# Kernel tuning notes

Measured on AMD Instinct MI355X. Metric: run time of the kernel, lower is better.

## Reference

```python
import jax, jax.numpy as jnp
import numpy as np

B, IN, H = 4096, 1024, 1024

def setup_inputs() -> dict:
    key = jax.random.key(0)
    ks = jax.random.split(key, 8)
    s = 1.0 / np.sqrt(IN + H)  # ~torch Linear init scale
    return {
        "x": jax.random.normal(ks[0], (B, IN), jnp.float32),
        "h_prev": jax.random.normal(ks[1], (B, H), jnp.float32),
        "c_prev": jax.random.normal(ks[2], (B, H), jnp.float32),
        "Wf": jax.random.normal(ks[3], (IN + H, H), jnp.float32) * s,
        "bf": jnp.zeros((H,), jnp.float32),
        "Wi": jax.random.normal(ks[4], (IN + H, H), jnp.float32) * s,
        "bi": jnp.zeros((H,), jnp.float32),
        "Wg": jax.random.normal(ks[5], (IN + H, H), jnp.float32) * s,
        "bg": jnp.zeros((H,), jnp.float32),
        "Wo": jax.random.normal(ks[6], (IN + H, H), jnp.float32) * s,
        "bo": jnp.zeros((H,), jnp.float32),
    }

def reference(x, h_prev, c_prev, Wf, bf, Wi, bi, Wg, bg, Wo, bo):
    combined = jnp.concatenate([x, h_prev], axis=1)          # [B, IN+H]
    # fuse the 4 gate projections into one GEMM: [B, IN+H] x [IN+H, 4H]
    W = jnp.concatenate([Wf, Wi, Wg, Wo], axis=1)            # [IN+H, 4H]
    b = jnp.concatenate([bf, bi, bg, bo], axis=0)            # [4H]
    gates = combined @ W + b                                  # [B, 4H]
    f_t, i_t, g_t, o_t = jnp.split(gates, 4, axis=1)
    f_t = jax.nn.sigmoid(f_t)
    i_t = jax.nn.sigmoid(i_t)
    g_t = jnp.tanh(g_t)
    o_t = jax.nn.sigmoid(o_t)
    c_next = f_t * c_prev + i_t * g_t
    h_next = o_t * jnp.tanh(c_next)
    return (h_next, c_next)
```

## Files before the change

### kernel.cpp

```cpp
#include <hip/hip_runtime.h>

#define B_DIM 4096
#define H_DIM 1024
#define K_DIM 2048
#define NTILE (K_DIM / 64)

typedef unsigned short u16;
typedef unsigned int u32;
typedef __attribute__((ext_vector_type(8))) short short8;
typedef __attribute__((ext_vector_type(4))) float f32x4;

typedef const __attribute__((address_space(1))) void* gas_ptr;
typedef __attribute__((address_space(3))) void* las_ptr;

#define WT_ELEMS (4 * H_DIM * K_DIM)
#define AC_ELEMS (B_DIM * K_DIM)
#define WS_NEEDED ((size_t)(WT_ELEMS + AC_ELEMS) * 2)

__device__ __forceinline__ void gl_lds16(const u16* g, u16* l) {
    __builtin_amdgcn_global_load_lds((gas_ptr)g, (las_ptr)l, 16, 0, 0);
}
__device__ __forceinline__ float bf2f(u16 v) {
    return __builtin_bit_cast(float, (u32)((u32)v << 16));
}
__device__ __forceinline__ u16 f2bf(float f) {
    u32 u = __builtin_bit_cast(u32, f);
    return (u16)((u + 0x7fffu + ((u >> 16) & 1u)) >> 16);
}
__device__ __forceinline__ float sigm(float x) { return 1.0f / (1.0f + __expf(-x)); }
__device__ __forceinline__ float tanh_f(float x) { return 1.0f - 2.0f / (__expf(2.0f * x) + 1.0f); }

__global__ __launch_bounds__(256) void prep_all(const float* __restrict__ x, const float* __restrict__ h,
                                                const float* __restrict__ Wf, const float* __restrict__ Wi,
                                                const float* __restrict__ Wg, const float* __restrict__ Wo,
                                                u16* __restrict__ A, u16* __restrict__ Wt) {
    const int t = threadIdx.x;
    if (blockIdx.x < 512) {
#pragma unroll
        for (int it = 0; it < 8; ++it) {
            int e = it * (512 * 256 * 8) + (blockIdx.x * 256 + t) * 8;
            int m = e >> 11, c = e & 2047;
            const float* src = (c < 1024) ? (x + (size_t)m * 1024 + c)
                                          : (h + (size_t)m * 1024 + (c - 1024));
            float4 v0 = ((const float4*)src)[0], v1 = ((const float4*)src)[1];
            short8 q;
            q[0] = (short)f2bf(v0.x); q[1] = (short)f2bf(v0.y); q[2] = (short)f2bf(v0.z); q[3] = (short)f2bf(v0.w);
            q[4] = (short)f2bf(v1.x); q[5] = (short)f2bf(v1.y); q[6] = (short)f2bf(v1.z); q[7] = (short)f2bf(v1.w);
            *(short8*)(A + e) = q;
        }
    } else {
        const int id = (blockIdx.x - 512) * 4 + (t >> 6);
        const int l = t & 63;
        const int k0 = (id & 31) * 64, n0 = ((id >> 5) & 15) * 64, g = id >> 9;
        const float* W = (g == 0) ? Wf : (g == 1) ? Wi : (g == 2) ? Wg : Wo;
        const int no = (l & 7) * 8;
        const int ko = (l >> 3) * 8;
        float f[8][8];
#pragma unroll
        for (int j = 0; j < 8; ++j) {
            const float4* s = (const float4*)(W + (size_t)(k0 + ko + j) * H_DIM + n0 + no);
            float4 a = s[0], b = s[1];
            f[j][0] = a.x; f[j][1] = a.y; f[j][2] = a.z; f[j][3] = a.w;
            f[j][4] = b.x; f[j][5] = b.y; f[j][6] = b.z; f[j][7] = b.w;
        }
        u16* dst0 = Wt + (size_t)g * ((size_t)H_DIM * K_DIM) + (size_t)(n0 + no) * K_DIM + k0 + ko;
#pragma unroll
        for (int w2 = 0; w2 < 8; ++w2) {
            short8 q;
#pragma unroll
            for (int j = 0; j < 8; ++j) q[j] = (short)f2bf(f[j][w2]);
            *(short8*)(dst0 + (size_t)w2 * K_DIM) = q;
        }
    }
}

#define PH_OPEN                                                  \
    __builtin_amdgcn_s_barrier();                                \
    __builtin_amdgcn_s_setprio(1)

#define PH_CLOSE                                                 \
    __builtin_amdgcn_s_setprio(0);                               \
    __builtin_amdgcn_s_barrier()

#define PH_CLOSE_VM2                                             \
    __builtin_amdgcn_s_setprio(0);                               \
    asm volatile("s_waitcnt vmcnt(2)" ::: "memory");             \
    __builtin_amdgcn_s_barrier()

#define PH_CLOSE_VM2_PIN                                         \
    __builtin_amdgcn_sched_barrier(0);                           \
    __builtin_amdgcn_s_setprio(0);                               \
    asm volatile("s_waitcnt vmcnt(2)" ::: "memory");             \
    __builtin_amdgcn_s_barrier()

#define PH_CLOSE_VM0                                             \
    __builtin_amdgcn_s_setprio(0);                               \
    asm volatile("s_waitcnt vmcnt(0)" ::: "memory");             \
    __builtin_amdgcn_s_barrier()

#define STG_A(NB, H)                                                              \
    gl_lds16(pa[H][0], &sm[NB][(H) * 8192 + t * 8]);        pa[H][0] += 64;       \
    gl_lds16(pa[H][1], &sm[NB][(H) * 8192 + 4096 + t * 8]); pa[H][1] += 64;

#define STG_B(NB, H)                                                                      \
    gl_lds16(pb[H][0], &sm[NB][16384 + (H) * 8192 + t * 8]);        pb[H][0] += 64;       \
    gl_lds16(pb[H][1], &sm[NB][16384 + (H) * 8192 + 4096 + t * 8]); pb[H][1] += 64;

#define RD_A(CB, KS)                                                                       \
    _Pragma("unroll") for (int mi = 0; mi < 8; ++mi)                                       \
        afr[mi] = *(const short8*)&sm[CB][(wr * 128 + mi * 16 + l15) * 64 +                \
                                          ((((KS) * 4 + quad) ^ v7) * 8)];

#define RD_B(CB, G, KS)                                                                    \
    (*(const short8*)&sm[CB][16384 + (G) * 4096 + (wc * 16 + l15) * 64 +                   \
                             ((((KS) * 4 + quad) ^ v7) * 8)])

#define MFMA_PAIR(GP)                                                                      \
    _Pragma("unroll") for (int mi = 0; mi < 8; ++mi)                                       \
        acc[mi][2 * (GP)] = __builtin_amdgcn_mfma_f32_16x16x32_bf16(                       \
            afr[mi], b0, acc[mi][2 * (GP)], 0, 0, 0);                                      \
    _Pragma("unroll") for (int mi = 0; mi < 8; ++mi)                                       \
        acc[mi][2 * (GP) + 1] = __builtin_amdgcn_mfma_f32_16x16x32_bf16(                   \
            afr[mi], b1, acc[mi][2 * (GP) + 1], 0, 0, 0);

__global__ __launch_bounds__(512, 2) void lstm_gemm(
    const u16* __restrict__ A, const u16* __restrict__ Wt, const float* __restrict__ c_prev,
    const float* __restrict__ bf_, const float* __restrict__ bi_,
    const float* __restrict__ bg_, const float* __restrict__ bo_,
    float* __restrict__ out) {
    __shared__ u16 sm[2][32768];

    const int t = threadIdx.x;
    const int w = t >> 6;
    const int l = t & 63;
    const int quad = l >> 4;
    const int l15 = l & 15;
    const int v7 = l15 & 7;
    const int wr = w >> 2;
    const int wc = w & 3;
    const int m0 = blockIdx.x * 256;
    const int j0 = blockIdx.y * 64;

    f32x4 acc[8][4];
#pragma unroll
    for (int mi = 0; mi < 8; ++mi)
#pragma unroll
        for (int g = 0; g < 4; ++g)
            acc[mi][g] = (f32x4){0.f, 0.f, 0.f, 0.f};

    const u16* pa[2][2];
    const u16* pb[2][2];
#pragma unroll
    for (int h = 0; h < 2; ++h)
#pragma unroll
        for (int i = 0; i < 2; ++i) {
            int e = h * 8192 + (i * 512 + t) * 8;
            int m = e >> 6, sl = (e >> 3) & 7;
            pa[h][i] = A + (size_t)(m0 + m) * K_DIM + ((sl ^ (m & 7)) * 8);
            int g = e >> 12, n = (e >> 6) & 63;
            pb[h][i] = Wt + (size_t)g * ((size_t)H_DIM * K_DIM) + (size_t)(j0 + n) * K_DIM +
                       ((sl ^ (n & 7)) * 8);
        }

    short8 afr[8], b0, b1;

    STG_A(0, 0); STG_A(0, 1); STG_B(0, 0); STG_B(0, 1);
    asm volatile("s_waitcnt vmcnt(2)" ::: "memory");
    __builtin_amdgcn_s_barrier();

    for (int kt = 0; kt < NTILE - 1; ++kt) {
        const int cb = kt & 1, nb = cb ^ 1;
        RD_A(cb, 0);
        b0 = RD_B(cb, 0, 0); b1 = RD_B(cb, 1, 0);
        STG_A(nb, 0);
        PH_OPEN;
        MFMA_PAIR(0);
        PH_CLOSE_VM2;
        b0 = RD_B(cb, 2, 0); b1 = RD_B(cb, 3, 0);
        STG_A(nb, 1);
        PH_OPEN;
        MFMA_PAIR(1);
        PH_CLOSE;
        RD_A(cb, 1);
        b0 = RD_B(cb, 0, 1); b1 = RD_B(cb, 1, 1);
        STG_B(nb, 0);
        PH_OPEN;
        MFMA_PAIR(0);
        PH_CLOSE;
        b0 = RD_B(cb, 2, 1); b1 = RD_B(cb, 3, 1);
        STG_B(nb, 1);
        PH_OPEN;
        MFMA_PAIR(1);
        PH_CLOSE_VM2_PIN;
    }
    {
        const int cb = (NTILE - 1) & 1;
        RD_A(cb, 0);
        b0 = RD_B(cb, 0, 0); b1 = RD_B(cb, 1, 0);
        PH_OPEN;
        MFMA_PAIR(0);
        PH_CLOSE_VM0;
        b0 = RD_B(cb, 2, 0); b1 = RD_B(cb, 3, 0);
        PH_OPEN;
        MFMA_PAIR(1);
        PH_CLOSE;
        RD_A(cb, 1);
        b0 = RD_B(cb, 0, 1); b1 = RD_B(cb, 1, 1);
        PH_OPEN;
        MFMA_PAIR(0);
        PH_CLOSE;
        b0 = RD_B(cb, 2, 1); b1 = RD_B(cb, 3, 1);
        MFMA_PAIR(1);
    }

    const int col = j0 + wc * 16 + l15;
    const float bF = bf_[col], bI = bi_[col], bG = bg_[col], bO = bo_[col];
#pragma unroll
    for (int mi = 0; mi < 8; ++mi) {
        const int rowbase = m0 + wr * 128 + mi * 16 + quad * 4;
        float cp[4];
#pragma unroll
        for (int rr = 0; rr < 4; ++rr)
            cp[rr] = c_prev[(size_t)(rowbase + rr) * H_DIM + col];
#pragma unroll
        for (int rr = 0; rr < 4; ++rr) {
            float fv = sigm(acc[mi][0][rr] + bF);
            float iv = sigm(acc[mi][1][rr] + bI);
            float gv = tanh_f(acc[mi][2][rr] + bG);
            float ov = sigm(acc[mi][3][rr] + bO);
            float cn = fv * cp[rr] + iv * gv;
            float hn = ov * tanh_f(cn);
            size_t idx = (size_t)(rowbase + rr) * H_DIM + col;
            out[idx] = hn;
            out[(size_t)B_DIM * H_DIM + idx] = cn;
        }
    }
}

__global__ __launch_bounds__(256) void lstm_f32(
    const float* __restrict__ x, const float* __restrict__ h_prev, const float* __restrict__ c_prev,
    const float* __restrict__ Wf, const float* __restrict__ Wi, const float* __restrict__ Wg, const float* __restrict__ Wo,
    const float* __restrict__ bf_, const float* __restrict__ bi_, const float* __restrict__ bg_, const float* __restrict__ bo_,
    float* __restrict__ out) {
    __shared__ u16 smem[16384];
    u16* sA = smem;
    u16* sB = smem + 4096;

    const int t = threadIdx.x;
    const int w = t >> 6;
    const int l = t & 63;
    const int quad = l >> 4;
    const int l15 = l & 15;
    const int wr = w >> 1;
    const int wc = w & 1;
    const int m0 = blockIdx.x * 128;
    const int j0 = blockIdx.y * 32;

    const int arow = t >> 1;
    const int akh = (t & 1) * 16;
    const int r7 = t & 127;
    const int bk = r7 >> 2;
    const int bn8 = (r7 & 3) * 8;
    const int kswz = ((((bk >> 3) ^ (bn8 >> 3)) << 3) | (bk & 7));
    const float* WpA = (t < 128) ? Wf : Wi;
    const float* WpB = (t < 128) ? Wg : Wo;
    const int gA = (t >> 7);
    const int gB = 2 + (t >> 7);

    f32x4 acc[2][4][2];
#pragma unroll
    for (int gi = 0; gi < 2; ++gi)
#pragma unroll
        for (int mi = 0; mi < 4; ++mi)
#pragma unroll
            for (int ni = 0; ni < 2; ++ni)
                acc[gi][mi][ni] = (f32x4){0.f, 0.f, 0.f, 0.f};

    for (int kt = 0; kt < K_DIM / 32; ++kt) {
        const float* srcA = (kt < 32) ? x : h_prev;
        const int koff = (kt & 31) * 32;
        __syncthreads();

        const float4* ap = (const float4*)(srcA + (size_t)(m0 + arow) * H_DIM + koff + akh);
        float4 a0 = ap[0], a1 = ap[1], a2 = ap[2], a3 = ap[3];
        short8 p0, p1;
        p0[0] = (short)f2bf(a0.x); p0[1] = (short)f2bf(a0.y); p0[2] = (short)f2bf(a0.z); p0[3] = (short)f2bf(a0.w);
        p0[4] = (short)f2bf(a1.x); p0[5] = (short)f2bf(a1.y); p0[6] = (short)f2bf(a1.z); p0[7] = (short)f2bf(a1.w);
        p1[0] = (short)f2bf(a2.x); p1[1] = (short)f2bf(a2.y); p1[2] = (short)f2bf(a2.z); p1[3] = (short)f2bf(a2.w);
        p1[4] = (short)f2bf(a3.x); p1[5] = (short)f2bf(a3.y); p1[6] = (short)f2bf(a3.z); p1[7] = (short)f2bf(a3.w);
        *(short8*)(sA + arow * 32 + akh) = p0;
        *(short8*)(sA + arow * 32 + akh + 8) = p1;

        const float* gpA = WpA + (size_t)(kt * 32 + bk) * H_DIM + j0 + bn8;
        const float* gpB = WpB + (size_t)(kt * 32 + bk) * H_DIM + j0 + bn8;
        float4 c0 = *(const float4*)gpA, c1 = *(const float4*)(gpA + 4);
        float4 d0 = *(const float4*)gpB, d1 = *(const float4*)(gpB + 4);
        sB[gA * 1024 + (bn8 + 0) * 32 + kswz] = f2bf(c0.x);
        sB[gA * 1024 + (bn8 + 1) * 32 + kswz] = f2bf(c0.y);
        sB[gA * 1024 + (bn8 + 2) * 32 + kswz] = f2bf(c0.z);
        sB[gA * 1024 + (bn8 + 3) * 32 + kswz] = f2bf(c0.w);
        sB[gA * 1024 + (bn8 + 4) * 32 + kswz] = f2bf(c1.x);
        sB[gA * 1024 + (bn8 + 5) * 32 + kswz] = f2bf(c1.y);
        sB[gA * 1024 + (bn8 + 6) * 32 + kswz] = f2bf(c1.z);
        sB[gA * 1024 + (bn8 + 7) * 32 + kswz] = f2bf(c1.w);
        sB[gB * 1024 + (bn8 + 0) * 32 + kswz] = f2bf(d0.x);
        sB[gB * 1024 + (bn8 + 1) * 32 + kswz] = f2bf(d0.y);
        sB[gB * 1024 + (bn8 + 2) * 32 + kswz] = f2bf(d0.z);
        sB[gB * 1024 + (bn8 + 3) * 32 + kswz] = f2bf(d0.w);
        sB[gB * 1024 + (bn8 + 4) * 32 + kswz] = f2bf(d1.x);
        sB[gB * 1024 + (bn8 + 5) * 32 + kswz] = f2bf(d1.y);
        sB[gB * 1024 + (bn8 + 6) * 32 + kswz] = f2bf(d1.z);
        sB[gB * 1024 + (bn8 + 7) * 32 + kswz] = f2bf(d1.w);
        __syncthreads();

        short8 bfr[2][2];
#pragma unroll
        for (int gi = 0; gi < 2; ++gi) {
            int g = wc * 2 + gi;
#pragma unroll
            for (int ni = 0; ni < 2; ++ni) {
                int n = ni * 16 + l15;
                bfr[gi][ni] = *(const short8*)(sB + g * 1024 + n * 32 + ((quad ^ (n >> 3)) * 8));
            }
        }
#pragma unroll
        for (int mi = 0; mi < 4; ++mi) {
            int m = wr * 64 + mi * 16 + l15;
            short8 afr = *(const short8*)(sA + m * 32 + quad * 8);
#pragma unroll
            for (int gi = 0; gi < 2; ++gi)
#pragma unroll
                for (int ni = 0; ni < 2; ++ni)
                    acc[gi][mi][ni] =
                        __builtin_amdgcn_mfma_f32_16x16x32_bf16(afr, bfr[gi][ni], acc[gi][mi][ni], 0, 0, 0);
        }
    }

    __syncthreads();
#pragma unroll
    for (int gi = 0; gi < 2; ++gi) {
        int g = wc * 2 + gi;
        const float* bp = (g == 0) ? bf_ : (g == 1) ? bi_ : (g == 2) ? bg_ : bo_;
#pragma unroll
        for (int ni = 0; ni < 2; ++ni) {
            int col = ni * 16 + l15;
            float bias = bp[j0 + col];
#pragma unroll
            for (int mi = 0; mi < 4; ++mi)
#pragma unroll
                for (int rr = 0; rr < 4; ++rr) {
                    int row = wr * 64 + mi * 16 + quad * 4 + rr;
                    float v = acc[gi][mi][ni][rr] + bias;
                    v = (g == 2) ? tanh_f(v) : sigm(v);
                    smem[g * 4096 + row * 32 + col] = f2bf(v);
                }
        }
    }
    __syncthreads();

    const int col = t & 31;
    const int rb = t >> 5;
#pragma unroll
    for (int p = 0; p < 16; ++p) {
        int row = p * 8 + rb;
        float fv = bf2f(smem[0 * 4096 + row * 32 + col]);
        float iv = bf2f(smem[1 * 4096 + row * 32 + col]);
        float gv = bf2f(smem[2 * 4096 + row * 32 + col]);
        float ov = bf2f(smem[3 * 4096 + row * 32 + col]);
        size_t oidx = (size_t)(m0 + row) * H_DIM + j0 + col;
        float cp = c_prev[oidx];
        float cn = fv * cp + iv * gv;
        float hn = ov * tanh_f(cn);
        out[oidx] = hn;
        out[(size_t)B_DIM * H_DIM + oidx] = cn;
    }
}

extern "C" void kernel_launch(void* const* d_in, const int* in_sizes, int n_in,
                              void* d_out, int out_size, void* d_ws, size_t ws_size,
                              hipStream_t stream) {
    const float* x   = (const float*)d_in[0];
    const float* hp  = (const float*)d_in[1];
    const float* cp  = (const float*)d_in[2];
    const float* Wf  = (const float*)d_in[3];
    const float* bf_ = (const float*)d_in[4];
    const float* Wi  = (const float*)d_in[5];
    const float* bi_ = (const float*)d_in[6];
    const float* Wg  = (const float*)d_in[7];
    const float* bg_ = (const float*)d_in[8];
    const float* Wo  = (const float*)d_in[9];
    const float* bo_ = (const float*)d_in[10];

    if (ws_size >= WS_NEEDED) {
        u16* Wt = (u16*)d_ws;
        u16* Ac = (u16*)d_ws + WT_ELEMS;
        prep_all<<<dim3(1024), dim3(256), 0, stream>>>(x, hp, Wf, Wi, Wg, Wo, Ac, Wt);
        lstm_gemm<<<dim3(B_DIM / 256, H_DIM / 64), dim3(512), 0, stream>>>(
            Ac, Wt, cp, bf_, bi_, bg_, bo_, (float*)d_out);
    } else {
        lstm_f32<<<dim3(B_DIM / 128, H_DIM / 32), dim3(256), 0, stream>>>(
            x, hp, cp, Wf, Wi, Wg, Wo, bf_, bi_, bg_, bo_, (float*)d_out);
    }
}
```

Before: 197.8 us.

## Switch gate GEMM to 32x32x16 MFMA with 4x2 wave layout

Replaces the 16x16x32 bf16 MFMA tiling (2x4 waves, each owning 128 rows by 16 columns per gate) with 32x32x16 MFMA tiles (4x2 waves, each owning 64 rows by 32 columns per gate). The LDS read addressing, the B staging pointer layout and the epilogue row mapping change to match the 32x32 accumulator layout. The aim is to cut LDS fragment reads per MFMA and issue fewer, larger matrix instructions. It shifts register pressure and LDS bank-access patterns, and the swizzle now keys on l&7 rather than l15&7.

Measured after the change: 207.3 us. 1.05x slower.

```diff
diff --git a/kernel.cpp b/kernel.cpp
--- a/kernel.cpp
+++ b/kernel.cpp
@@ -9,6 +9,7 @@
 typedef unsigned int u32;
 typedef __attribute__((ext_vector_type(8))) short short8;
 typedef __attribute__((ext_vector_type(4))) float f32x4;
+typedef __attribute__((ext_vector_type(16))) float f32x16;
 
 typedef const __attribute__((address_space(1))) void* gas_ptr;
 typedef __attribute__((address_space(3))) void* las_ptr;
@@ -106,22 +107,26 @@
     gl_lds16(pb[H][0], &sm[NB][16384 + (H) * 8192 + t * 8]);        pb[H][0] += 64;       \
     gl_lds16(pb[H][1], &sm[NB][16384 + (H) * 8192 + 4096 + t * 8]); pb[H][1] += 64;
 
-#define RD_A(CB, KS)                                                                       \
-    _Pragma("unroll") for (int mi = 0; mi < 8; ++mi)                                       \
-        afr[mi] = *(const short8*)&sm[CB][(wr * 128 + mi * 16 + l15) * 64 +                \
-                                          ((((KS) * 4 + quad) ^ v7) * 8)];
-
-#define RD_B(CB, G, KS)                                                                    \
-    (*(const short8*)&sm[CB][16384 + (G) * 4096 + (wc * 16 + l15) * 64 +                   \
-                             ((((KS) * 4 + quad) ^ v7) * 8)])
-
-#define MFMA_PAIR(GP)                                                                      \
-    _Pragma("unroll") for (int mi = 0; mi < 8; ++mi)                                       \
-        acc[mi][2 * (GP)] = __builtin_amdgcn_mfma_f32_16x16x32_bf16(                       \
-            afr[mi], b0, acc[mi][2 * (GP)], 0, 0, 0);                                      \
-    _Pragma("unroll") for (int mi = 0; mi < 8; ++mi)                                       \
-        acc[mi][2 * (GP) + 1] = __builtin_amdgcn_mfma_f32_16x16x32_bf16(                   \
-            afr[mi], b1, acc[mi][2 * (GP) + 1], 0, 0, 0);
+#define RD_A32(CB, KH)                                                                     \
+    _Pragma("unroll") for (int mt = 0; mt < 2; ++mt)                                       \
+    _Pragma("unroll") for (int ks = 0; ks < 2; ++ks)                                       \
+        afr[mt * 2 + ks] = *(const short8*)&sm[CB][(wr * 64 + mt * 32 + l31) * 64 +        \
+                                                   (((KH) * 4 + ks * 2 + hi) ^ v7) * 8];
+
+#define RD_B32(CB, GP, GL, KH)                                                             \
+    _Pragma("unroll") for (int ks = 0; ks < 2; ++ks)                                       \
+        bfr[(GL) * 2 + ks] = *(const short8*)&sm[CB][16384 +                               \
+            (((GP) * 2 + (GL)) * 2 + wc) * 2048 + l31 * 64 +                               \
+            (((KH) * 4 + ks * 2 + hi) ^ v7) * 8];
+
+#define MFMA_Q(GP)                                                                         \
+    _Pragma("unroll") for (int mt = 0; mt < 2; ++mt)                                       \
+    _Pragma("unroll") for (int ks = 0; ks < 2; ++ks) {                                     \
+        acc[mt][2 * (GP)]     = __builtin_amdgcn_mfma_f32_32x32x16_bf16(                   \
+            afr[mt * 2 + ks], bfr[0 * 2 + ks], acc[mt][2 * (GP)], 0, 0, 0);                \
+        acc[mt][2 * (GP) + 1] = __builtin_amdgcn_mfma_f32_32x32x16_bf16(                   \
+            afr[mt * 2 + ks], bfr[1 * 2 + ks], acc[mt][2 * (GP) + 1], 0, 0, 0);            \
+    }
 
 __global__ __launch_bounds__(512, 2) void lstm_gemm(
     const u16* __restrict__ A, const u16* __restrict__ Wt, const float* __restrict__ c_prev,
@@ -133,20 +138,21 @@
     const int t = threadIdx.x;
     const int w = t >> 6;
     const int l = t & 63;
-    const int quad = l >> 4;
-    const int l15 = l & 15;
-    const int v7 = l15 & 7;
-    const int wr = w >> 2;
-    const int wc = w & 3;
+    const int l31 = l & 31;
+    const int hi = l >> 5;
+    const int v7 = l & 7;
+    const int wr = w >> 1;
+    const int wc = w & 1;
     const int m0 = blockIdx.x * 256;
     const int j0 = blockIdx.y * 64;
 
-    f32x4 acc[8][4];
-#pragma unroll
-    for (int mi = 0; mi < 8; ++mi)
+    f32x16 acc[2][4];
+#pragma unroll
+    for (int mt = 0; mt < 2; ++mt)
 #pragma unroll
         for (int g = 0; g < 4; ++g)
-            acc[mi][g] = (f32x4){0.f, 0.f, 0.f, 0.f};
+            acc[mt][g] = (f32x16){0.f, 0.f, 0.f, 0.f, 0.f, 0.f, 0.f, 0.f,
+                                  0.f, 0.f, 0.f, 0.f, 0.f, 0.f, 0.f, 0.f};
 
     const u16* pa[2][2];
     const u16* pb[2][2];
@@ -157,12 +163,13 @@
             int e = h * 8192 + (i * 512 + t) * 8;
             int m = e >> 6, sl = (e >> 3) & 7;
             pa[h][i] = A + (size_t)(m0 + m) * K_DIM + ((sl ^ (m & 7)) * 8);
-            int g = e >> 12, n = (e >> 6) & 63;
-            pb[h][i] = Wt + (size_t)g * ((size_t)H_DIM * K_DIM) + (size_t)(j0 + n) * K_DIM +
-                       ((sl ^ (n & 7)) * 8);
-        }
-
-    short8 afr[8], b0, b1;
+            int nt = e >> 11, c = (e >> 6) & 31;
+            int g = nt >> 1, hh = nt & 1;
+            pb[h][i] = Wt + (size_t)g * ((size_t)H_DIM * K_DIM) +
+                       (size_t)(j0 + hh * 32 + c) * K_DIM + ((sl ^ (c & 7)) * 8);
+        }
+
+    short8 afr[4], bfr[4];
 
     STG_A(0, 0); STG_A(0, 1); STG_B(0, 0); STG_B(0, 1);
     asm volatile("s_waitcnt vmcnt(2)" ::: "memory");
@@ -170,67 +177,65 @@
 
     for (int kt = 0; kt < NTILE - 1; ++kt) {
         const int cb = kt & 1, nb = cb ^ 1;
-        RD_A(cb, 0);
-        b0 = RD_B(cb, 0, 0); b1 = RD_B(cb, 1, 0);
+        RD_A32(cb, 0);
+        RD_B32(cb, 0, 0, 0); RD_B32(cb, 0, 1, 0);
         STG_A(nb, 0);
         PH_OPEN;
-        MFMA_PAIR(0);
+        MFMA_Q(0);
         PH_CLOSE_VM2;
-        b0 = RD_B(cb, 2, 0); b1 = RD_B(cb, 3, 0);
+        RD_B32(cb, 1, 0, 0); RD_B32(cb, 1, 1, 0);
         STG_A(nb, 1);
         PH_OPEN;
-        MFMA_PAIR(1);
+        MFMA_Q(1);
         PH_CLOSE;
-        RD_A(cb, 1);
-        b0 = RD_B(cb, 0, 1); b1 = RD_B(cb, 1, 1);
+        RD_A32(cb, 1);
+        RD_B32(cb, 0, 0, 1); RD_B32(cb, 0, 1, 1);
         STG_B(nb, 0);
         PH_OPEN;
-        MFMA_PAIR(0);
+        MFMA_Q(0);
         PH_CLOSE;
-        b0 = RD_B(cb, 2, 1); b1 = RD_B(cb, 3, 1);
+        RD_B32(cb, 1, 0, 1); RD_B32(cb, 1, 1, 1);
         STG_B(nb, 1);
         PH_OPEN;
-        MFMA_PAIR(1);
+        MFMA_Q(1);
         PH_CLOSE_VM2_PIN;
     }
     {
         const int cb = (NTILE - 1) & 1;
-        RD_A(cb, 0);
-        b0 = RD_B(cb, 0, 0); b1 = RD_B(cb, 1, 0);
-        PH_OPEN;
-        MFMA_PAIR(0);
+        RD_A32(cb, 0);
+        RD_B32(cb, 0, 0, 0); RD_B32(cb, 0, 1, 0);
+        PH_OPEN;
+        MFMA_Q(0);
         PH_CLOSE_VM0;
-        b0 = RD_B(cb, 2, 0); b1 = RD_B(cb, 3, 0);
-        PH_OPEN;
-        MFMA_PAIR(1);
+        RD_B32(cb, 1, 0, 0); RD_B32(cb, 1, 1, 0);
+        PH_OPEN;
+        MFMA_Q(1);
         PH_CLOSE;
-        RD_A(cb, 1);
-        b0 = RD_B(cb, 0, 1); b1 = RD_B(cb, 1, 1);
-        PH_OPEN;
-        MFMA_PAIR(0);
+        RD_A32(cb, 1);
+        RD_B32(cb, 0, 0, 1); RD_B32(cb, 0, 1, 1);
+        PH_OPEN;
+        MFMA_Q(0);
         PH_CLOSE;
-        b0 = RD_B(cb, 2, 1); b1 = RD_B(cb, 3, 1);
-        MFMA_PAIR(1);
-    }
-
-    const int col = j0 + wc * 16 + l15;
+        RD_B32(cb, 1, 0, 1); RD_B32(cb, 1, 1, 1);
+        MFMA_Q(1);
+    }
+
+    const int col = j0 + wc * 32 + l31;
     const float bF = bf_[col], bI = bi_[col], bG = bg_[col], bO = bo_[col];
 #pragma unroll
-    for (int mi = 0; mi < 8; ++mi) {
-        const int rowbase = m0 + wr * 128 + mi * 16 + quad * 4;
-        float cp[4];
-#pragma unroll
-        for (int rr = 0; rr < 4; ++rr)
-            cp[rr] = c_prev[(size_t)(rowbase + rr) * H_DIM + col];
-#pragma unroll
-        for (int rr = 0; rr < 4; ++rr) {
-            float fv = sigm(acc[mi][0][rr] + bF);
-            float iv = sigm(acc[mi][1][rr] + bI);
-            float gv = tanh_f(acc[mi][2][rr] + bG);
-            float ov = sigm(acc[mi][3][rr] + bO);
-            float cn = fv * cp[rr] + iv * gv;
+    for (int mt = 0; mt < 2; ++mt) {
+        const int rb0 = m0 + wr * 64 + mt * 32 + hi * 4;
+#pragma unroll
+        for (int r = 0; r < 16; ++r) {
+            const int row = rb0 + (r & 3) + 8 * (r >> 2);
+            size_t idx = (size_t)row * H_DIM + col;
+            float cpv = c_prev[idx];
+            float fv = sigm(acc[mt][0][r] + bF);
+            float iv = sigm(acc[mt][1][r] + bI);
+            float gv = tanh_f(acc[mt][2][r] + bG);
+            float ov = sigm(acc[mt][3][r] + bO);
+            float cn = fv * cpv + iv * gv;
             float hn = ov * tanh_f(cn);
-            size_t idx = (size_t)(rowbase + rr) * H_DIM + col;
             out[idx] = hn;
             out[(size_t)B_DIM * H_DIM + idx] = cn;
         }
```
